# Kernel optimization log

Measured on AMD Instinct MI355X. Metric: run time of the kernel, lower is better.

## Reference

```python
import jax, jax.numpy as jnp
import numpy as np

N_NODES = 100000
D_IN = 64
HID = 128
N_EDGES = 1600000
N_LBL = 500000


def setup_inputs() -> dict:
    key = jax.random.key(0)
    ks = jax.random.split(key, 16)
    s = 0.05
    return {
        "x": jax.random.normal(ks[0], (N_NODES, D_IN), dtype=jnp.float32),
        "edge_index": jax.random.randint(ks[1], (2, N_EDGES), 0, N_NODES, dtype=jnp.int64),
        "edge_label_index": jax.random.randint(ks[2], (2, N_LBL), 0, N_NODES, dtype=jnp.int64),
        # SAGEConv1: lin_l (aggregated neighbors, with bias), lin_r (root, no bias)
        "w1l": jax.random.normal(ks[3], (D_IN, HID), dtype=jnp.float32) * s,
        "b1l": jnp.zeros((HID,), dtype=jnp.float32),
        "w1r": jax.random.normal(ks[4], (D_IN, HID), dtype=jnp.float32) * s,
        # SAGEConv2
        "w2l": jax.random.normal(ks[5], (HID, HID), dtype=jnp.float32) * s,
        "b2l": jnp.zeros((HID,), dtype=jnp.float32),
        "w2r": jax.random.normal(ks[6], (HID, HID), dtype=jnp.float32) * s,
        # EdgeDecoder
        "dw1": jax.random.normal(ks[7], (2 * HID, HID), dtype=jnp.float32) * s,
        "db1": jnp.zeros((HID,), dtype=jnp.float32),
        "dw2": jax.random.normal(ks[8], (HID, 1), dtype=jnp.float32) * s,
        "db2": jnp.zeros((1,), dtype=jnp.float32),
    }


def _sage_conv(x, src, dst, inv_deg, wl, bl, wr):
    # mean-aggregate neighbor features at destination nodes, then linear
    agg = jax.ops.segment_sum(x[src], dst, num_segments=N_NODES)  # [N, d]
    mean = agg * inv_deg[:, None]
    return mean @ wl + bl + x @ wr


def reference(x, edge_index, edge_label_index,
              w1l, b1l, w1r, w2l, b2l, w2r, dw1, db1, dw2, db2):
    src, dst = edge_index[0], edge_index[1]
    deg = jax.ops.segment_sum(jnp.ones((N_EDGES,), jnp.float32), dst,
                              num_segments=N_NODES)
    inv_deg = jnp.where(deg > 0, 1.0 / jnp.maximum(deg, 1.0), 0.0)

    # encoder: SAGEConv -> relu -> SAGEConv
    h = jax.nn.relu(_sage_conv(x, src, dst, inv_deg, w1l, b1l, w1r))
    z = _sage_conv(h, src, dst, inv_deg, w2l, b2l, w2r)  # [N, HID]

    # decoder: gather endpoint embeddings per label edge, concat, MLP
    zz = jnp.concatenate([z[edge_label_index[0]], z[edge_label_index[1]]],
                         axis=-1)  # [E_lbl, 2*HID]
    h2 = jax.nn.relu(zz @ dw1 + db1)
    out = h2 @ dw2 + db2  # [E_lbl, 1]
    return out.reshape(-1)
```

## Files before the change

kernel.cpp:

```cpp
#include <hip/hip_runtime.h>

#define N_NODES 100000
#define D_IN 64
#define HID 128
#define N_EDGES 1600000
#define N_LBL 500000
#define NBUCK 196
#define NSCANB 98
#define LCAP 3072

typedef __attribute__((ext_vector_type(8))) short bf16x8;
typedef __attribute__((ext_vector_type(4))) float f32x4;

__device__ inline unsigned short f2bf(float f) {
  unsigned int u = __float_as_uint(f);
  return (unsigned short)((u + 0x7FFFu + ((u >> 16) & 1u)) >> 16);
}
__device__ inline float bf_lo(unsigned int w) { return __uint_as_float(w << 16); }
__device__ inline float bf_hi(unsigned int w) { return __uint_as_float(w & 0xFFFF0000u); }
__device__ inline float bfs(short s) {
  return __uint_as_float(((unsigned int)(unsigned short)s) << 16);
}

__global__ __launch_bounds__(256) void k_deg(const int* __restrict__ dst,
                                             int* __restrict__ deg) {
  int e = blockIdx.x * 256 + threadIdx.x;
  if (e < N_EDGES) atomicAdd(&deg[dst[e]], 1);
}

__global__ __launch_bounds__(1024) void k_scan_a(const int* __restrict__ deg,
                                                 int* __restrict__ rowptr,
                                                 float* __restrict__ inv,
                                                 int* __restrict__ bsum) {
  __shared__ int s_wsum[16];
  const int lane = threadIdx.x & 63;
  const int wid = threadIdx.x >> 6;
  const int i = blockIdx.x * 1024 + threadIdx.x;
  int v = (i < N_NODES) ? deg[i] : 0;
  int x = v;
#pragma unroll
  for (int off = 1; off < 64; off <<= 1) {
    int t = __shfl_up(x, off);
    if (lane >= off) x += t;
  }
  if (lane == 63) s_wsum[wid] = x;
  __syncthreads();
  if (wid == 0 && lane < 16) {
    int ws = s_wsum[lane];
    int y = ws;
#pragma unroll
    for (int off = 1; off < 16; off <<= 1) {
      int t = __shfl_up(y, off);
      if (lane >= off) y += t;
    }
    s_wsum[lane] = y - ws;
    if (lane == 15) bsum[blockIdx.x] = y;
  }
  __syncthreads();
  if (i < N_NODES) {
    rowptr[i] = s_wsum[wid] + x - v;
    inv[i] = v > 0 ? 1.0f / (float)v : 0.0f;
  }
}

__global__ __launch_bounds__(128) void k_scan_b(int* __restrict__ bsum,
                                                int* __restrict__ rowptr) {
  __shared__ int s_w;
  const int tid = threadIdx.x;
  const int lane = tid & 63, wid = tid >> 6;
  int v = (tid < NSCANB) ? bsum[tid] : 0;
  int x = v;
#pragma unroll
  for (int off = 1; off < 64; off <<= 1) {
    int t = __shfl_up(x, off);
    if (lane >= off) x += t;
  }
  if (wid == 0 && lane == 63) s_w = x;
  __syncthreads();
  int incl = x + (wid == 1 ? s_w : 0);
  if (tid < NSCANB) bsum[tid] = incl - v;
  if (tid == NSCANB - 1) rowptr[N_NODES] = incl;
}

__global__ __launch_bounds__(1024) void k_scan_c(int* __restrict__ rowptr,
                                                 const int* __restrict__ bsum,
                                                 int* __restrict__ gcursor) {
  const int i = blockIdx.x * 1024 + threadIdx.x;
  if (i < N_NODES) {
    int r = rowptr[i] + bsum[blockIdx.x];
    rowptr[i] = r;
    if ((i & 511) == 0) gcursor[i >> 9] = r;
  }
}

__global__ __launch_bounds__(256) void k_bin(const int* __restrict__ src,
                                             const int* __restrict__ dst,
                                             int* __restrict__ gcursor,
                                             int* __restrict__ binned) {
  __shared__ int hist[NBUCK];
  __shared__ int base[NBUCK];
  const int tid = threadIdx.x;
  const int e0 = blockIdx.x * 4096 + tid;
  for (int t = tid; t < NBUCK; t += 256) hist[t] = 0;
  __syncthreads();

  int w[16], bk[16], rk[16];
#pragma unroll
  for (int i = 0; i < 16; ++i) {
    int e = e0 + i * 256;
    if (e < N_EDGES) {
      int s = src[e], d = dst[e];
      bk[i] = d >> 9;
      w[i] = (s << 9) | (d & 511);
      rk[i] = atomicAdd(&hist[bk[i]], 1);
    } else {
      bk[i] = -1;
    }
  }
  __syncthreads();
  for (int t = tid; t < NBUCK; t += 256)
    base[t] = hist[t] > 0 ? atomicAdd(&gcursor[t], hist[t]) : 0;
  __syncthreads();
#pragma unroll
  for (int i = 0; i < 16; ++i)
    if (bk[i] >= 0) binned[base[bk[i]] + rk[i]] = w[i];
}

__global__ __launch_bounds__(256) void k_fill2(const int* __restrict__ rowptr,
                                               const int* __restrict__ binned,
                                               int* __restrict__ csr) {
  __shared__ int lcur[512];
  const int b = blockIdx.x;
  const int nb = b << 9;
  const int nn = min(512, N_NODES - nb);
  for (int i = threadIdx.x; i < nn; i += 256) lcur[i] = rowptr[nb + i];
  __syncthreads();
  const int beg = rowptr[nb], end = rowptr[nb + nn];
  for (int e = beg + threadIdx.x; e < end; e += 256) {
    int w = binned[e];
    int pos = atomicAdd(&lcur[w & 511], 1);
    csr[pos] = w >> 9;
  }
}

__global__ __launch_bounds__(256) void k_lbl_bin(const int* __restrict__ ls,
                                                 const int* __restrict__ ld,
                                                 int* __restrict__ lblcnt,
                                                 int2* __restrict__ lbin) {
  __shared__ int hist[NBUCK];
  __shared__ int base[NBUCK];
  const int tid = threadIdx.x;
  const int e0 = blockIdx.x * 4096 + tid;
  for (int t = tid; t < NBUCK; t += 256) hist[t] = 0;
  __syncthreads();

  int dd[16], pk[16], bk[16], rk[16];
#pragma unroll
  for (int i = 0; i < 16; ++i) {
    int e = e0 + i * 256;
    if (e < N_LBL) {
      int s = ls[e];
      dd[i] = ld[e];
      bk[i] = s >> 9;
      pk[i] = (e << 9) | (s & 511);
      rk[i] = atomicAdd(&hist[bk[i]], 1);
    } else {
      bk[i] = -1;
    }
  }
  __syncthreads();
  for (int t = tid; t < NBUCK; t += 256)
    base[t] = hist[t] > 0 ? atomicAdd(&lblcnt[t], hist[t]) : 0;
  __syncthreads();
#pragma unroll
  for (int i = 0; i < 16; ++i)
    if (bk[i] >= 0) {
      int2 rec = {dd[i], pk[i]};
      lbin[(long)bk[i] * LCAP + base[bk[i]] + rk[i]] = rec;
    }
}

__global__ __launch_bounds__(256) void k_prep(
    const float* __restrict__ x, const float* __restrict__ w1l,
    const float* __restrict__ w1r,
    unsigned short* __restrict__ x16, unsigned short* __restrict__ w1lt,
    unsigned short* __restrict__ w1rt) {
  long gid = (long)blockIdx.x * 256 + threadIdx.x;
  if (gid < 1600000) {
    long i = gid * 4;
    float4 v = *(const float4*)&x[i];
    ushort4 q = {f2bf(v.x), f2bf(v.y), f2bf(v.z), f2bf(v.w)};
    *(ushort4*)&x16[i] = q;
    return;
  }
  long idx = gid - 1600000;
  if (idx < 8192) { int n = idx >> 6, k = idx & 63; w1lt[idx] = f2bf(w1l[k * 128 + n]); return; }
  idx -= 8192;
  if (idx < 8192) { int n = idx >> 6, k = idx & 63; w1rt[idx] = f2bf(w1r[k * 128 + n]); }
}

__global__ __launch_bounds__(256) void k_prepw(
    const float* __restrict__ w2l, const float* __restrict__ w2r,
    const float* __restrict__ dw1, const float* __restrict__ b2l,
    const float* __restrict__ db1,
    unsigned short* __restrict__ Wt, float* __restrict__ buv) {
  int idx = blockIdx.x * 256 + threadIdx.x;
  if (idx < 65536) {
    int mat = idx >> 14;
    int rem = idx & 16383;
    int k = rem >> 7;
    int n = rem & 127;
    const float* w = (mat & 1) ? w2r : w2l;
    const float* d = dw1 + (mat >> 1) * (128 * 128);
    float acc = 0.f;
#pragma unroll 8
    for (int j = 0; j < 128; ++j) acc = fmaf(w[k * 128 + j], d[j * 128 + n], acc);
    Wt[(long)mat * 16384 + n * 128 + k] = f2bf(acc);
  } else if (idx < 65792) {
    int t = idx - 65536;
    int n = t & 127;
    const float* d = dw1 + (t >> 7) * (128 * 128);
    float acc = (t < 128) ? db1[n] : 0.f;
#pragma unroll 8
    for (int j = 0; j < 128; ++j) acc = fmaf(b2l[j], d[j * 128 + n], acc);
    buv[t] = acc;
  }
}

__global__ __launch_bounds__(256) void k_agg64(const int* __restrict__ rowptr,
                                               const int* __restrict__ csr,
                                               const unsigned short* __restrict__ f16,
                                               const float* __restrict__ inv,
                                               unsigned short* __restrict__ out16) {
  const int lane = threadIdx.x & 63;
  const int n = blockIdx.x * 4 + (threadIdx.x >> 6);
  const int beg = rowptr[n], end = rowptr[n + 1];
  float acc = 0.0f;
  int j = beg;
  for (; j + 4 <= end; j += 4) {
    int s0 = csr[j], s1 = csr[j + 1], s2 = csr[j + 2], s3 = csr[j + 3];
    float f0 = bf_lo((unsigned int)f16[(long)s0 * 64 + lane]);
    float f1 = bf_lo((unsigned int)f16[(long)s1 * 64 + lane]);
    float f2 = bf_lo((unsigned int)f16[(long)s2 * 64 + lane]);
    float f3 = bf_lo((unsigned int)f16[(long)s3 * 64 + lane]);
    acc += f0; acc += f1; acc += f2; acc += f3;
  }
  for (; j < end; ++j) acc += bf_lo((unsigned int)f16[(long)csr[j] * 64 + lane]);
  out16[(long)n * 64 + lane] = f2bf(acc * inv[n]);
}

__global__ __launch_bounds__(256) void k_agg128(const int* __restrict__ rowptr,
                                                const int* __restrict__ csr,
                                                const unsigned short* __restrict__ f16,
                                                const float* __restrict__ inv,
                                                unsigned short* __restrict__ out16) {
  const int lane = threadIdx.x & 63;
  const int wv = threadIdx.x >> 6;
  const int g = lane >> 4;
  const int q = lane & 15;
  const int n = (blockIdx.x * 4 + wv) * 4 + g;
  const int beg = rowptr[n], end = rowptr[n + 1];
  float acc[8] = {0, 0, 0, 0, 0, 0, 0, 0};
  int j = beg;
  for (; j + 2 <= end; j += 2) {
    int s0 = csr[j], s1 = csr[j + 1];
    bf16x8 v0 = *(const bf16x8*)(f16 + (long)s0 * 128 + q * 8);
    bf16x8 v1 = *(const bf16x8*)(f16 + (long)s1 * 128 + q * 8);
#pragma unroll
    for (int i = 0; i < 8; ++i) acc[i] += bfs(v0[i]);
#pragma unroll
    for (int i = 0; i < 8; ++i) acc[i] += bfs(v1[i]);
  }
  if (j < end) {
    bf16x8 v0 = *(const bf16x8*)(f16 + (long)csr[j] * 128 + q * 8);
#pragma unroll
    for (int i = 0; i < 8; ++i) acc[i] += bfs(v0[i]);
  }
  float iv = inv[n];
  bf16x8 r;
#pragma unroll
  for (int i = 0; i < 8; ++i) r[i] = (short)f2bf(acc[i] * iv);
  *(bf16x8*)(out16 + (long)n * 128 + q * 8) = r;
}

__global__ __launch_bounds__(256) void k_l1(
    const unsigned short* __restrict__ m1, const unsigned short* __restrict__ x16,
    const unsigned short* __restrict__ w1lt, const unsigned short* __restrict__ w1rt,
    const float* __restrict__ b1l, unsigned short* __restrict__ h16) {
  const int l = threadIdx.x & 63;
  const int w = threadIdx.x >> 6;
  const int cl = l & 15;
  const int kh = l >> 4;
  const int wrow0 = blockIdx.x * 128 + w * 32;
  int ar0 = wrow0 + cl;      if (ar0 >= N_NODES) ar0 = N_NODES - 1;
  int ar1 = wrow0 + 16 + cl; if (ar1 >= N_NODES) ar1 = N_NODES - 1;

  f32x4 acc[2][8];
#pragma unroll
  for (int t = 0; t < 2; ++t)
#pragma unroll
    for (int nt = 0; nt < 8; ++nt) acc[t][nt] = (f32x4){0.f, 0.f, 0.f, 0.f};

#pragma unroll
  for (int s = 0; s < 2; ++s) {
    const int ko = s * 32 + kh * 8;
    bf16x8 am0 = *(const bf16x8*)(m1 + (long)ar0 * 64 + ko);
    bf16x8 ax0 = *(const bf16x8*)(x16 + (long)ar0 * 64 + ko);
    bf16x8 am1 = *(const bf16x8*)(m1 + (long)ar1 * 64 + ko);
    bf16x8 ax1 = *(const bf16x8*)(x16 + (long)ar1 * 64 + ko);
#pragma unroll
    for (int nt = 0; nt < 8; ++nt) {
      bf16x8 bl = *(const bf16x8*)(w1lt + (long)(nt * 16 + cl) * 64 + ko);
      bf16x8 br = *(const bf16x8*)(w1rt + (long)(nt * 16 + cl) * 64 + ko);
      acc[0][nt] = __builtin_amdgcn_mfma_f32_16x16x32_bf16(am0, bl, acc[0][nt], 0, 0, 0);
      acc[0][nt] = __builtin_amdgcn_mfma_f32_16x16x32_bf16(ax0, br, acc[0][nt], 0, 0, 0);
      acc[1][nt] = __builtin_amdgcn_mfma_f32_16x16x32_bf16(am1, bl, acc[1][nt], 0, 0, 0);
      acc[1][nt] = __builtin_amdgcn_mfma_f32_16x16x32_bf16(ax1, br, acc[1][nt], 0, 0, 0);
    }
  }

#pragma unroll
  for (int t = 0; t < 2; ++t)
#pragma unroll
    for (int nt = 0; nt < 8; ++nt) {
      float b = b1l[nt * 16 + cl];
#pragma unroll
      for (int i = 0; i < 4; ++i) {
        int r = wrow0 + t * 16 + kh * 4 + i;
        if (r < N_NODES)
          h16[(long)r * 128 + nt * 16 + cl] = f2bf(fmaxf(acc[t][nt][i] + b, 0.0f));
      }
    }
}

__global__ __launch_bounds__(128) void k_uv(
    const unsigned short* __restrict__ m2, const unsigned short* __restrict__ h16,
    const unsigned short* __restrict__ Wt, const float* __restrict__ buv,
    unsigned short* __restrict__ u16, unsigned short* __restrict__ v16) {
  const int l = threadIdx.x & 63;
  const int w = threadIdx.x >> 6;
  const int cl = l & 15;
  const int kh = l >> 4;
  const int row0 = blockIdx.x * 32;
  const int ar0 = row0 + cl;
  const int ar1 = row0 + 16 + cl;
  const unsigned short* Wm = Wt + (long)(w ? 2 : 0) * 16384;
  const unsigned short* Wh = Wt + (long)(w ? 3 : 1) * 16384;

  f32x4 acc[2][8];
#pragma unroll
  for (int t = 0; t < 2; ++t)
#pragma unroll
    for (int nt = 0; nt < 8; ++nt) acc[t][nt] = (f32x4){0.f, 0.f, 0.f, 0.f};

#pragma unroll
  for (int s = 0; s < 4; ++s) {
    const int ko = s * 32 + kh * 8;
    bf16x8 am0 = *(const bf16x8*)(m2 + (long)ar0 * 128 + ko);
    bf16x8 ah0 = *(const bf16x8*)(h16 + (long)ar0 * 128 + ko);
    bf16x8 am1 = *(const bf16x8*)(m2 + (long)ar1 * 128 + ko);
    bf16x8 ah1 = *(const bf16x8*)(h16 + (long)ar1 * 128 + ko);
#pragma unroll
    for (int nt = 0; nt < 8; ++nt) {
      bf16x8 bm = *(const bf16x8*)(Wm + (long)(nt * 16 + cl) * 128 + ko);
      bf16x8 bh = *(const bf16x8*)(Wh + (long)(nt * 16 + cl) * 128 + ko);
      acc[0][nt] = __builtin_amdgcn_mfma_f32_16x16x32_bf16(am0, bm, acc[0][nt], 0, 0, 0);
      acc[0][nt] = __builtin_amdgcn_mfma_f32_16x16x32_bf16(ah0, bh, acc[0][nt], 0, 0, 0);
      acc[1][nt] = __builtin_amdgcn_mfma_f32_16x16x32_bf16(am1, bm, acc[1][nt], 0, 0, 0);
      acc[1][nt] = __builtin_amdgcn_mfma_f32_16x16x32_bf16(ah1, bh, acc[1][nt], 0, 0, 0);
    }
  }

  unsigned short* outp = w ? v16 : u16;
#pragma unroll
  for (int t = 0; t < 2; ++t)
#pragma unroll
    for (int nt = 0; nt < 8; ++nt) {
      float bb = buv[w * 128 + nt * 16 + cl];
#pragma unroll
      for (int i = 0; i < 4; ++i) {
        int r = row0 + t * 16 + kh * 4 + i;
        outp[(long)r * 128 + nt * 16 + cl] = f2bf(acc[t][nt][i] + bb);
      }
    }
}

__global__ __launch_bounds__(256) void k_edge2(
    const int* __restrict__ lblcnt, const int2* __restrict__ lbin,
    const unsigned short* __restrict__ u16, const unsigned short* __restrict__ v16,
    const float* __restrict__ dw2, const float* __restrict__ db2,
    float* __restrict__ out) {
  const int lane = threadIdx.x & 63;
  const int wv = threadIdx.x >> 6;
  const int g = lane >> 4;
  const int q = lane & 15;
  const int b = blockIdx.x / (LCAP / 16);
  const int chunk = blockIdx.x % (LCAP / 16);
  const int idx = chunk * 16 + wv * 4 + g;
  if (idx >= lblcnt[b]) return;
  int2 rec = lbin[(long)b * LCAP + idx];
  int d = rec.x;
  int s = (b << 9) + (rec.y & 511);
  int e = rec.y >> 9;

  bf16x8 uu = *(const bf16x8*)(u16 + (long)s * 128 + q * 8);
  bf16x8 vv = *(const bf16x8*)(v16 + (long)d * 128 + q * 8);
  float4 w0 = *(const float4*)&dw2[q * 8];
  float4 w1 = *(const float4*)&dw2[q * 8 + 4];
  float w8[8] = {w0.x, w0.y, w0.z, w0.w, w1.x, w1.y, w1.z, w1.w};
  float sum = 0.0f;
#pragma unroll
  for (int i = 0; i < 8; ++i) {
    float h = fmaxf(bfs(uu[i]) + bfs(vv[i]), 0.0f);
    sum = fmaf(h, w8[i], sum);
  }
  sum += __shfl_xor(sum, 1);
  sum += __shfl_xor(sum, 2);
  sum += __shfl_xor(sum, 4);
  sum += __shfl_xor(sum, 8);
  if (q == 0) out[e] = sum + db2[0];
}

extern "C" void kernel_launch(void* const* d_in, const int* in_sizes, int n_in,
                              void* d_out, int out_size, void* d_ws, size_t ws_size,
                              hipStream_t stream) {
  const float* x   = (const float*)d_in[0];
  const int*   ei  = (const int*)d_in[1];
  const int*   eli = (const int*)d_in[2];
  const float* w1l = (const float*)d_in[3];
  const float* b1l = (const float*)d_in[4];
  const float* w1r = (const float*)d_in[5];
  const float* w2l = (const float*)d_in[6];
  const float* b2l = (const float*)d_in[7];
  const float* w2r = (const float*)d_in[8];
  const float* dw1 = (const float*)d_in[9];
  const float* db1 = (const float*)d_in[10];
  const float* dw2 = (const float*)d_in[11];
  const float* db2 = (const float*)d_in[12];
  float* out = (float*)d_out;

  char* wsb = (char*)d_ws;
  float* inv     = (float*)(wsb + 0);
  int*   deg_i   = (int*)(wsb + 400000);
  int*   rowptr  = (int*)(wsb + 800000);
  int*   gcursor = (int*)(wsb + 1200032);
  int*   csr     = (int*)(wsb + 1201056);
  int*   binned  = (int*)(wsb + 7601056);
  unsigned short* x16  = (unsigned short*)(wsb + 14001056);
  unsigned short* m1   = (unsigned short*)(wsb + 26801056);
  unsigned short* u16  = (unsigned short*)(wsb + 14001056);
  unsigned short* h16  = (unsigned short*)(wsb + 39601056);
  unsigned short* m2   = (unsigned short*)(wsb + 65201056);
  unsigned short* v16  = (unsigned short*)(wsb + 90801056);
  unsigned short* w1lt = (unsigned short*)(wsb + 116401056);
  unsigned short* w1rt = (unsigned short*)(wsb + 116417440);
  unsigned short* Wt   = (unsigned short*)(wsb + 116433824);
  float* buv     = (float*)(wsb + 116564896);
  int*   bsum    = (int*)(wsb + 116565920);
  int*   lblcnt  = (int*)(wsb + 116566432);
  int2*  lbin    = (int2*)(wsb + 116567456);

  const int* srcp = ei;
  const int* dstp = ei + N_EDGES;
  const int* lsp  = eli;
  const int* ldp  = eli + N_LBL;

  hipMemsetAsync(deg_i, 0, N_NODES * sizeof(int), stream);
  hipMemsetAsync(lblcnt, 0, NBUCK * sizeof(int), stream);
  k_deg<<<N_EDGES / 256, 256, 0, stream>>>(dstp, deg_i);
  k_scan_a<<<NSCANB, 1024, 0, stream>>>(deg_i, rowptr, inv, bsum);
  k_scan_b<<<1, 128, 0, stream>>>(bsum, rowptr);
  k_scan_c<<<NSCANB, 1024, 0, stream>>>(rowptr, bsum, gcursor);
  k_bin<<<(N_EDGES + 4095) / 4096, 256, 0, stream>>>(srcp, dstp, gcursor, binned);
  k_fill2<<<NBUCK, 256, 0, stream>>>(rowptr, binned, csr);
  k_lbl_bin<<<(N_LBL + 4095) / 4096, 256, 0, stream>>>(lsp, ldp, lblcnt, lbin);
  k_prep<<<(1616384 + 255) / 256, 256, 0, stream>>>(x, w1l, w1r, x16, w1lt, w1rt);
  k_prepw<<<257, 256, 0, stream>>>(w2l, w2r, dw1, b2l, db1, Wt, buv);

  k_agg64<<<N_NODES / 4, 256, 0, stream>>>(rowptr, csr, x16, inv, m1);
  k_l1<<<(N_NODES + 127) / 128, 256, 0, stream>>>(m1, x16, w1lt, w1rt, b1l, h16);

  k_agg128<<<N_NODES / 16, 256, 0, stream>>>(rowptr, csr, h16, inv, m2);
  k_uv<<<N_NODES / 32, 128, 0, stream>>>(m2, h16, Wt, buv, u16, v16);

  k_edge2<<<NBUCK * (LCAP / 16), 256, 0, stream>>>(lblcnt, lbin, u16, v16, dw2, db2, out);
}
```

Baseline: 444.9 us.

## Split neighbor lists across lane groups in aggregation kernels with shuffle reduction

Both mean-aggregation kernels now assign one node per wavefront, with lane groups each taking a strided subset of the node's neighbors and loading 16-byte bf16x8 vectors. Partial sums are combined with xor shuffles, and one lane group writes the result. In k_agg64 this replaces per-lane 2-byte loads with vector loads and gives 8 independent neighbor streams per wave. In k_agg128 it gives 4 concurrent neighbor rows per node instead of 4 nodes per wave, meant to raise memory-level parallelism and reduce degree-imbalance divergence, at the cost of shuffle reductions and 4x more blocks.

Measured after the change: 423.1 us. -4.9%, faster.

```diff
diff --git a/kernel.cpp b/kernel.cpp
--- a/kernel.cpp
+++ b/kernel.cpp
@@ -233,20 +233,38 @@
                                                const float* __restrict__ inv,
                                                unsigned short* __restrict__ out16) {
   const int lane = threadIdx.x & 63;
-  const int n = blockIdx.x * 4 + (threadIdx.x >> 6);
+  const int wv = threadIdx.x >> 6;
+  const int q = lane & 7;
+  const int g = lane >> 3;
+  const int n = blockIdx.x * 4 + wv;
   const int beg = rowptr[n], end = rowptr[n + 1];
-  float acc = 0.0f;
-  int j = beg;
-  for (; j + 4 <= end; j += 4) {
-    int s0 = csr[j], s1 = csr[j + 1], s2 = csr[j + 2], s3 = csr[j + 3];
-    float f0 = bf_lo((unsigned int)f16[(long)s0 * 64 + lane]);
-    float f1 = bf_lo((unsigned int)f16[(long)s1 * 64 + lane]);
-    float f2 = bf_lo((unsigned int)f16[(long)s2 * 64 + lane]);
-    float f3 = bf_lo((unsigned int)f16[(long)s3 * 64 + lane]);
-    acc += f0; acc += f1; acc += f2; acc += f3;
-  }
-  for (; j < end; ++j) acc += bf_lo((unsigned int)f16[(long)csr[j] * 64 + lane]);
-  out16[(long)n * 64 + lane] = f2bf(acc * inv[n]);
+  float acc[8] = {0, 0, 0, 0, 0, 0, 0, 0};
+  int j = beg + g;
+  for (; j + 8 < end; j += 16) {
+    int s0 = csr[j], s1 = csr[j + 8];
+    bf16x8 v0 = *(const bf16x8*)(f16 + (long)s0 * 64 + q * 8);
+    bf16x8 v1 = *(const bf16x8*)(f16 + (long)s1 * 64 + q * 8);
+#pragma unroll
+    for (int i = 0; i < 8; ++i) acc[i] += bfs(v0[i]);
+#pragma unroll
+    for (int i = 0; i < 8; ++i) acc[i] += bfs(v1[i]);
+  }
+  if (j < end) {
+    bf16x8 v0 = *(const bf16x8*)(f16 + (long)csr[j] * 64 + q * 8);
+#pragma unroll
+    for (int i = 0; i < 8; ++i) acc[i] += bfs(v0[i]);
+  }
+#pragma unroll
+  for (int m = 8; m <= 32; m <<= 1)
+#pragma unroll
+    for (int i = 0; i < 8; ++i) acc[i] += __shfl_xor(acc[i], m);
+  if (g == 0) {
+    float iv = inv[n];
+    bf16x8 r;
+#pragma unroll
+    for (int i = 0; i < 8; ++i) r[i] = (short)f2bf(acc[i] * iv);
+    *(bf16x8*)(out16 + (long)n * 64 + q * 8) = r;
+  }
 }
 
 __global__ __launch_bounds__(256) void k_agg128(const int* __restrict__ rowptr,
@@ -256,14 +274,14 @@
                                                 unsigned short* __restrict__ out16) {
   const int lane = threadIdx.x & 63;
   const int wv = threadIdx.x >> 6;
+  const int q = lane & 15;
   const int g = lane >> 4;
-  const int q = lane & 15;
-  const int n = (blockIdx.x * 4 + wv) * 4 + g;
+  const int n = blockIdx.x * 4 + wv;
   const int beg = rowptr[n], end = rowptr[n + 1];
   float acc[8] = {0, 0, 0, 0, 0, 0, 0, 0};
-  int j = beg;
-  for (; j + 2 <= end; j += 2) {
-    int s0 = csr[j], s1 = csr[j + 1];
+  int j = beg + g;
+  for (; j + 4 < end; j += 8) {
+    int s0 = csr[j], s1 = csr[j + 4];
     bf16x8 v0 = *(const bf16x8*)(f16 + (long)s0 * 128 + q * 8);
     bf16x8 v1 = *(const bf16x8*)(f16 + (long)s1 * 128 + q * 8);
 #pragma unroll
@@ -276,11 +294,17 @@
 #pragma unroll
     for (int i = 0; i < 8; ++i) acc[i] += bfs(v0[i]);
   }
-  float iv = inv[n];
-  bf16x8 r;
-#pragma unroll
-  for (int i = 0; i < 8; ++i) r[i] = (short)f2bf(acc[i] * iv);
-  *(bf16x8*)(out16 + (long)n * 128 + q * 8) = r;
+#pragma unroll
+  for (int m = 16; m <= 32; m <<= 1)
+#pragma unroll
+    for (int i = 0; i < 8; ++i) acc[i] += __shfl_xor(acc[i], m);
+  if (g == 0) {
+    float iv = inv[n];
+    bf16x8 r;
+#pragma unroll
+    for (int i = 0; i < 8; ++i) r[i] = (short)f2bf(acc[i] * iv);
+    *(bf16x8*)(out16 + (long)n * 128 + q * 8) = r;
+  }
 }
 
 __global__ __launch_bounds__(256) void k_l1(
@@ -480,7 +504,7 @@
   k_agg64<<<N_NODES / 4, 256, 0, stream>>>(rowptr, csr, x16, inv, m1);
   k_l1<<<(N_NODES + 127) / 128, 256, 0, stream>>>(m1, x16, w1lt, w1rt, b1l, h16);
 
-  k_agg128<<<N_NODES / 16, 256, 0, stream>>>(rowptr, csr, h16, inv, m2);
+  k_agg128<<<N_NODES / 4, 256, 0, stream>>>(rowptr, csr, h16, inv, m2);
   k_uv<<<N_NODES / 32, 128, 0, stream>>>(m2, h16, Wt, buv, u16, v16);
 
   k_edge2<<<NBUCK * (LCAP / 16), 256, 0, stream>>>(lblcnt, lbin, u16, v16, dw2, db2, out);
```
